# Optimization experiments

Hardware: AMD Instinct MI355X
Metric: run time of the kernel (lower is better)

## Reference

```python
import jax, jax.numpy as jnp
import numpy as np

B, N, K = 4, 2048, 32
CIN, COUT, M = 64, 64, 8
HID = 16
EPS = 1e-5


def setup_inputs() -> dict:
    key = jax.random.key(0)
    ks = jax.random.split(key, 12)
    inp = {
        "grouped_xyz": jax.random.normal(ks[0], (B, 3, N, K), jnp.float32),
        "grouped_dist": jax.random.uniform(ks[1], (B, N, K), jnp.float32),
        "grouped_norm": jax.random.normal(ks[2], (B, 3, N, K), jnp.float32),
        "grouped_angle": jax.random.normal(ks[3], (B, 3, N, K), jnp.float32),
        "feature": jax.random.normal(ks[4], (B, CIN, N, K), jnp.float32),
        # scorenet conv1 (14->16, 1x1, no bias) + BN params
        "w1": jax.random.normal(ks[5], (HID, 14), jnp.float32) * (2.0 / 14) ** 0.5,
        "g1": jnp.ones((HID,), jnp.float32),
        "b1": jnp.zeros((HID,), jnp.float32),
        # scorenet conv2 (16->M, 1x1, with bias, no last bn)
        "w2": jax.random.normal(ks[6], (M, HID), jnp.float32) * (2.0 / HID) ** 0.5,
        "bias2": jnp.zeros((M,), jnp.float32),
        # weight bank: kaiming on (M, CIN, COUT) -> permute -> (CIN, M*COUT)
        "weightbank": (jax.random.normal(ks[7], (M, CIN, COUT), jnp.float32)
                       * (2.0 / CIN) ** 0.5).transpose(1, 0, 2).reshape(CIN, M * COUT),
        # output BN params
        "gamma": jnp.ones((COUT,), jnp.float32),
        "beta": jnp.zeros((COUT,), jnp.float32),
    }
    return inp


def _bn_train(x, gamma, beta):
    # BatchNorm2d in training mode: stats over (B, N, K) per channel (axis=1)
    mean = x.mean(axis=(0, 2, 3), keepdims=True)
    var = x.var(axis=(0, 2, 3), keepdims=True)
    xn = (x - mean) * jax.lax.rsqrt(var + EPS)
    return xn * gamma[None, :, None, None] + beta[None, :, None, None]


def _softmax_one(x, axis):
    # exp(x) / (1 + sum exp(x)), numerically stable
    m = jax.lax.stop_gradient(x.max(axis=axis, keepdims=True))
    e = jnp.exp(x - m)
    return e / (e.sum(axis=axis, keepdims=True) + jnp.exp(-m))


def reference(grouped_xyz, grouped_dist, grouped_norm, grouped_angle, feature,
              w1, g1, b1, w2, bias2, weightbank, gamma, beta):
    # geometric feature build -> (B, 14, N, K)
    center_norm = jnp.broadcast_to(grouped_norm[..., :1], grouped_norm.shape)
    norm_diff = grouped_norm - center_norm
    norm_ed = jnp.linalg.norm(norm_diff, axis=1, keepdims=True)   # (B,1,N,K)
    xyz_ed = jnp.linalg.norm(grouped_xyz, axis=1, keepdims=True)  # (B,1,N,K)
    xyz = jnp.concatenate(
        [grouped_xyz, xyz_ed, grouped_norm, norm_diff, norm_ed, grouped_angle],
        axis=1) / (1.0 + grouped_dist[:, None, :, :])

    # scorenet: 1x1 conv + BN + ReLU, then 1x1 conv + bias, softmax_one over channels
    h = jnp.einsum('oc,bcnk->bonk', w1, xyz)
    h = jax.nn.relu(_bn_train(h, g1, b1))
    s = jnp.einsum('oc,bcnk->bonk', w2, h) + bias2[None, :, None, None]
    scores = _softmax_one(s, axis=1)                 # (B, M, N, K)
    scores = scores.transpose(0, 2, 3, 1)            # (B, N, K, M)

    # weight-bank matmul + score-weighted combine
    feat = feature.transpose(0, 2, 3, 1)             # (B, N, K, CIN)
    out = (feat @ weightbank).reshape(B, N, K, M, COUT)
    out = jnp.einsum('bnkm,bnkmo->bnko', scores, out)  # (B, N, K, COUT)
    out = out.transpose(0, 3, 1, 2)                  # (B, COUT, N, K)

    out = _bn_train(out, gamma, beta)
    return jax.nn.relu(out)
```

## Files before the change

kernel.cpp:

```cpp
#include <hip/hip_runtime.h>
#include <hip/hip_bf16.h>
#include <math.h>

namespace {

constexpr int Kn   = 32;
constexpr int CIN  = 64;
constexpr int COUT = 64;
constexpr int Mn   = 8;
constexpr int HIDn = 16;
constexpr int NK   = 65536;
constexpr int PTOT = 262144;
constexpr float EPSf = 1e-5f;

constexpr int NBLK = 256;
constexpr int NTHR = 1024;

constexpr int WS_SUM1 = 0;
constexpr int WS_SQ1  = 16;
constexpr int WS_SUM2 = 64;
constexpr int WS_SQ2  = 128;
constexpr int WS_BAR  = 192;
constexpr int WS_TOT  = 256;

typedef short bf16x8  __attribute__((ext_vector_type(8)));
typedef float f32x4   __attribute__((ext_vector_type(4)));
typedef float f32x16  __attribute__((ext_vector_type(16)));

__device__ __forceinline__ short f2bf(float f) {
  union { __hip_bfloat16 h; unsigned short u; } cv;
  cv.h = __float2bfloat16(f);
  return (short)cv.u;
}

__device__ __forceinline__ float ws_ld(const float* p) {
  return __hip_atomic_load(p, __ATOMIC_RELAXED, __HIP_MEMORY_SCOPE_AGENT);
}

__device__ __forceinline__ void gridbar(int* cnt, int tid, int target) {
  __syncthreads();
  if (tid == 0) {
    __hip_atomic_fetch_add(cnt, 1, __ATOMIC_ACQ_REL, __HIP_MEMORY_SCOPE_AGENT);
    while (__hip_atomic_load(cnt, __ATOMIC_ACQUIRE,
                             __HIP_MEMORY_SCOPE_AGENT) < target) {
      __builtin_amdgcn_s_sleep(8);
    }
  }
  __syncthreads();
}

__device__ __forceinline__ void geom_h(
    const float* __restrict__ xyz, const float* __restrict__ dist,
    const float* __restrict__ nrm, const float* __restrict__ ang,
    const float* __restrict__ w1, int b, int rem, float h[HIDn]) {
  const int cbase = rem & ~(Kn - 1);
  float x[14];
  const float invd = 1.0f / (1.0f + dist[b * NK + rem]);
  float xe = 0.f, ne = 0.f;
#pragma unroll
  for (int d = 0; d < 3; ++d) {
    const int base = (b * 3 + d) * NK;
    const float gx = xyz[base + rem];
    const float gn = nrm[base + rem];
    const float cn = nrm[base + cbase];
    const float ga = ang[base + rem];
    const float nd = gn - cn;
    x[d] = gx; x[4 + d] = gn; x[7 + d] = nd; x[11 + d] = ga;
    xe += gx * gx; ne += nd * nd;
  }
  x[3]  = sqrtf(xe);
  x[10] = sqrtf(ne);
#pragma unroll
  for (int i = 0; i < 14; ++i) x[i] *= invd;
#pragma unroll
  for (int o = 0; o < HIDn; ++o) {
    float s = 0.f;
#pragma unroll
    for (int c = 0; c < 14; ++c) s = fmaf(w1[o * 14 + c], x[c], s);
    h[o] = s;
  }
}

__global__ __launch_bounds__(512) void k0_zero(float* __restrict__ ws) {
  if (threadIdx.x < WS_TOT) ws[threadIdx.x] = 0.f;
}

__global__ __launch_bounds__(NTHR, 1) void kmain(
    const float* __restrict__ xyz, const float* __restrict__ dist,
    const float* __restrict__ nrm, const float* __restrict__ ang,
    const float* __restrict__ feature, const float* __restrict__ w1,
    const float* __restrict__ g1, const float* __restrict__ b1,
    const float* __restrict__ w2, const float* __restrict__ bias2,
    const float* __restrict__ wb, const float* __restrict__ gamma,
    const float* __restrict__ beta, float* __restrict__ ws,
    float* __restrict__ out) {
  __shared__ short lds_b[64 * 64 * 8];
  __shared__ unsigned park[16 * NTHR];
  __shared__ float red[16][128];
  __shared__ float bnp[160];

  int* const bar = (int*)(ws + WS_BAR);

  const int tid = threadIdx.x;
  const int l   = tid & 63;
  const int w   = tid >> 6;
  const int lg  = l >> 5;
  const int col = l & 31;

  const int blk = blockIdx.x;
  const int pos = blk * NTHR + tid;
  const int b   = pos >> 16;
  const int rem = pos & (NK - 1);

#pragma unroll
  for (int ff = 0; ff < 4; ++ff) {
    const int fi = w * 4 + ff;
    const int kk = fi >> 1;
    const int ct = fi & 1;
    const int c  = kk * 2 + lg;
    const int o  = ct * 32 + col;
    bf16x8 frag;
#pragma unroll
    for (int j = 0; j < 8; ++j) frag[j] = f2bf(wb[c * 512 + j * 64 + o]);
    *reinterpret_cast<bf16x8*>(&lds_b[(fi * 64 + l) * 8]) = frag;
  }

  float h[HIDn];
  geom_h(xyz, dist, nrm, ang, w1, b, rem, h);
  {
    float v[32];
#pragma unroll
    for (int i = 0; i < 16; ++i) { v[i] = h[i]; v[16 + i] = h[i] * h[i]; }
#pragma unroll
    for (int off = 32; off >= 1; off >>= 1) {
#pragma unroll
      for (int i = 0; i < 32; ++i) v[i] += __shfl_xor(v[i], off);
    }
    float mv = 0.f;
#pragma unroll
    for (int i = 0; i < 32; ++i) { if (l == i) mv = v[i]; }
    if (l < 32) red[w][l] = mv;
    __syncthreads();
    if (tid < 32) {
      float tot = 0.f;
#pragma unroll
      for (int ww = 0; ww < 16; ++ww) tot += red[ww][tid];
      atomicAdd(&ws[WS_SUM1 + tid], tot);
    }
  }

  gridbar(bar, tid, NBLK);

  if (tid < HIDn) {
    const float inv  = 1.0f / (float)PTOT;
    const float mean = ws_ld(&ws[WS_SUM1 + tid]) * inv;
    const float var  = ws_ld(&ws[WS_SQ1 + tid]) * inv - mean * mean;
    const float s    = g1[tid] * rsqrtf(var + EPSf);
    bnp[tid]      = s;
    bnp[16 + tid] = b1[tid] - mean * s;
  }
  __syncthreads();

  unsigned scp[4];
  {
#pragma unroll
    for (int o = 0; o < HIDn; ++o)
      h[o] = fmaxf(fmaf(h[o], bnp[o], bnp[16 + o]), 0.f);
    float s[Mn];
#pragma unroll
    for (int m = 0; m < Mn; ++m) {
      float a = bias2[m];
#pragma unroll
      for (int j = 0; j < HIDn; ++j) a = fmaf(w2[m * HIDn + j], h[j], a);
      s[m] = a;
    }
    float mx = s[0];
#pragma unroll
    for (int m = 1; m < Mn; ++m) mx = fmaxf(mx, s[m]);
    float sc[Mn];
    float ssum = 0.f;
#pragma unroll
    for (int m = 0; m < Mn; ++m) { sc[m] = expf(s[m] - mx); ssum += sc[m]; }
    const float inv = 1.0f / (ssum + expf(-mx));
#pragma unroll
    for (int m = 0; m < Mn; ++m) sc[m] *= inv;
#pragma unroll
    for (int j = 0; j < 4; ++j) {
      scp[j] = (unsigned)(unsigned short)f2bf(sc[2 * j]) |
               ((unsigned)(unsigned short)f2bf(sc[2 * j + 1]) << 16);
    }
  }

  const int wrem = (blk * NTHR + w * 64) & (NK - 1);
  const float* fbase = feature + (size_t)b * CIN * NK + wrem;
  f32x16 acc0, acc1;

#pragma unroll
  for (int grp = 0; grp < 2; ++grp) {
    unsigned s0p[4];
#pragma unroll
    for (int j = 0; j < 4; ++j) s0p[j] = __shfl(scp[j], grp * 32 + col);
#pragma unroll
    for (int i = 0; i < 16; ++i) { acc0[i] = 0.f; acc1[i] = 0.f; }

    const float* fp = fbase + (size_t)lg * NK + grp * 32 + col;
#pragma unroll 4
    for (int kk = 0; kk < 32; ++kk) {
      const float fA = *fp;
      fp += 2 * NK;
      bf16x8 a;
#pragma unroll
      for (int j = 0; j < 4; ++j) {
        const float slo = __uint_as_float(s0p[j] << 16);
        const float shi = __uint_as_float(s0p[j] & 0xffff0000u);
        a[2 * j]     = f2bf(fA * slo);
        a[2 * j + 1] = f2bf(fA * shi);
      }
      const bf16x8 b0 =
          *reinterpret_cast<const bf16x8*>(&lds_b[((kk * 2 + 0) * 64 + l) * 8]);
      const bf16x8 b1 =
          *reinterpret_cast<const bf16x8*>(&lds_b[((kk * 2 + 1) * 64 + l) * 8]);
      acc0 = __builtin_amdgcn_mfma_f32_32x32x16_bf16(a, b0, acc0, 0, 0, 0);
      acc1 = __builtin_amdgcn_mfma_f32_32x32x16_bf16(a, b1, acc1, 0, 0, 0);
    }

    {
      float s0s = 0.f, q0s = 0.f, s1s = 0.f, q1s = 0.f;
#pragma unroll
      for (int i = 0; i < 16; ++i) {
        s0s += acc0[i]; q0s += acc0[i] * acc0[i];
        s1s += acc1[i]; q1s += acc1[i] * acc1[i];
      }
      s0s += __shfl_xor(s0s, 32); q0s += __shfl_xor(q0s, 32);
      s1s += __shfl_xor(s1s, 32); q1s += __shfl_xor(q1s, 32);
      if (l < 32) {
        if (grp == 0) {
          red[w][col]      = s0s; red[w][32 + col] = s1s;
          red[w][64 + col] = q0s; red[w][96 + col] = q1s;
        } else {
          red[w][col]      += s0s; red[w][32 + col] += s1s;
          red[w][64 + col] += q0s; red[w][96 + col] += q1s;
        }
      }
    }

    if (grp == 0) {
#pragma unroll
      for (int i = 0; i < 8; ++i) {
        const unsigned w0 =
            (unsigned)(unsigned short)f2bf(acc0[2 * i]) |
            ((unsigned)(unsigned short)f2bf(acc0[2 * i + 1]) << 16);
        const unsigned w1 =
            (unsigned)(unsigned short)f2bf(acc1[2 * i]) |
            ((unsigned)(unsigned short)f2bf(acc1[2 * i + 1]) << 16);
        park[i * NTHR + tid]       = w0;
        park[(8 + i) * NTHR + tid] = w1;
      }
    }
  }

  __syncthreads();
  if (tid < 128) {
    float tot = 0.f;
#pragma unroll
    for (int ww = 0; ww < 16; ++ww) tot += red[ww][tid];
    atomicAdd(&ws[WS_SUM2 + tid], tot);
  }

  gridbar(bar, tid, 2 * NBLK);

  if (tid < COUT) {
    const float inv  = 1.0f / (float)PTOT;
    const float mean = ws_ld(&ws[WS_SUM2 + tid]) * inv;
    const float var  = ws_ld(&ws[WS_SQ2 + tid]) * inv - mean * mean;
    const float s    = gamma[tid] * rsqrtf(var + EPSf);
    bnp[32 + tid] = s;
    bnp[96 + tid] = beta[tid] - mean * s;
  }
  __syncthreads();

  float* obase = out + (size_t)b * COUT * NK + wrem;
#pragma unroll
  for (int ct = 0; ct < 2; ++ct) {
    const int o = ct * 32 + col;
    const float scl = bnp[32 + o];
    const float sh  = bnp[96 + o];
    float* orow = obase + (size_t)o * NK;
#pragma unroll
    for (int q = 0; q < 4; ++q) {
      f32x4 v1;
#pragma unroll
      for (int i = 0; i < 4; ++i) {
        const float vv = ct ? acc1[q * 4 + i] : acc0[q * 4 + i];
        v1[i] = fmaxf(fmaf(vv, scl, sh), 0.f);
      }
      *reinterpret_cast<f32x4*>(&orow[32 + q * 8 + 4 * lg]) = v1;
      const unsigned wa = park[(ct * 8 + q * 2 + 0) * NTHR + tid];
      const unsigned wb2 = park[(ct * 8 + q * 2 + 1) * NTHR + tid];
      f32x4 v0;
      v0[0] = __uint_as_float(wa << 16);
      v0[1] = __uint_as_float(wa & 0xffff0000u);
      v0[2] = __uint_as_float(wb2 << 16);
      v0[3] = __uint_as_float(wb2 & 0xffff0000u);
#pragma unroll
      for (int i = 0; i < 4; ++i) v0[i] = fmaxf(fmaf(v0[i], scl, sh), 0.f);
      *reinterpret_cast<f32x4*>(&orow[q * 8 + 4 * lg]) = v0;
    }
  }
}

}

extern "C" void kernel_launch(void* const* d_in, const int* in_sizes, int n_in,
                              void* d_out, int out_size, void* d_ws, size_t ws_size,
                              hipStream_t stream) {
  const float* xyz     = (const float*)d_in[0];
  const float* dist    = (const float*)d_in[1];
  const float* nrm     = (const float*)d_in[2];
  const float* ang     = (const float*)d_in[3];
  const float* feature = (const float*)d_in[4];
  const float* w1      = (const float*)d_in[5];
  const float* g1      = (const float*)d_in[6];
  const float* b1      = (const float*)d_in[7];
  const float* w2      = (const float*)d_in[8];
  const float* bias2   = (const float*)d_in[9];
  const float* wb      = (const float*)d_in[10];
  const float* gamma   = (const float*)d_in[11];
  const float* beta    = (const float*)d_in[12];
  float* out = (float*)d_out;
  float* ws  = (float*)d_ws;

  hipLaunchKernelGGL(k0_zero, dim3(1), dim3(512), 0, stream, ws);
  hipLaunchKernelGGL(kmain, dim3(NBLK), dim3(NTHR), 0, stream,
                     xyz, dist, nrm, ang, feature, w1, g1, b1,
                     w2, bias2, wb, gamma, beta, ws, out);
}
```

Before: 84.24 us.

## Replicate grid-barrier counters and BN stat slots; stage output stores through LDS

Batch-norm statistics and the grid-barrier counter are spread over 8 replicas, chosen by block index. This cuts contention on single atomic addresses, at the cost of summing the replicas after each barrier. Output tiles are written into a per-wave padded LDS staging buffer, then read back transposed, so each store instruction writes 32 consecutive floats of one output row instead of scattered 16-byte chunks. Shared memory becomes one manually carved buffer, and the staging area reuses the weight and reduction regions once they are no longer needed. The f32x4 writes into the stride-33 staging buffer may not be 16-byte aligned.

```diff
diff --git a/kernel.cpp b/kernel.cpp
--- a/kernel.cpp
+++ b/kernel.cpp
@@ -15,13 +15,9 @@
 
 constexpr int NBLK = 256;
 constexpr int NTHR = 1024;
-
-constexpr int WS_SUM1 = 0;
-constexpr int WS_SQ1  = 16;
-constexpr int WS_SUM2 = 64;
-constexpr int WS_SQ2  = 128;
-constexpr int WS_BAR  = 192;
-constexpr int WS_TOT  = 256;
+constexpr int NREP = 8;
+
+constexpr int WS_ZERO = 4096;
 
 typedef short bf16x8  __attribute__((ext_vector_type(8)));
 typedef float f32x4   __attribute__((ext_vector_type(4)));
@@ -37,14 +33,22 @@
   return __hip_atomic_load(p, __ATOMIC_RELAXED, __HIP_MEMORY_SCOPE_AGENT);
 }
 
-__device__ __forceinline__ void gridbar(int* cnt, int tid, int target) {
+__device__ __forceinline__ void gridbar(float* ws, int blk, int tid,
+                                        int target) {
+  int* cnt = (int*)(ws + 2048);
   __syncthreads();
   if (tid == 0) {
-    __hip_atomic_fetch_add(cnt, 1, __ATOMIC_ACQ_REL, __HIP_MEMORY_SCOPE_AGENT);
-    while (__hip_atomic_load(cnt, __ATOMIC_ACQUIRE,
-                             __HIP_MEMORY_SCOPE_AGENT) < target) {
-      __builtin_amdgcn_s_sleep(8);
-    }
+    __hip_atomic_fetch_add(&cnt[(blk & (NREP - 1)) * 16], 1, __ATOMIC_ACQ_REL,
+                           __HIP_MEMORY_SCOPE_AGENT);
+    int s;
+    do {
+      s = 0;
+#pragma unroll
+      for (int i = 0; i < NREP; ++i)
+        s += __hip_atomic_load(&cnt[i * 16], __ATOMIC_ACQUIRE,
+                               __HIP_MEMORY_SCOPE_AGENT);
+      if (s < target) __builtin_amdgcn_s_sleep(8);
+    } while (s < target);
   }
   __syncthreads();
 }
@@ -82,7 +86,7 @@
 }
 
 __global__ __launch_bounds__(512) void k0_zero(float* __restrict__ ws) {
-  if (threadIdx.x < WS_TOT) ws[threadIdx.x] = 0.f;
+  for (int i = threadIdx.x; i < WS_ZERO; i += 512) ws[i] = 0.f;
 }
 
 __global__ __launch_bounds__(NTHR, 1) void kmain(
@@ -94,12 +98,11 @@
     const float* __restrict__ wb, const float* __restrict__ gamma,
     const float* __restrict__ beta, float* __restrict__ ws,
     float* __restrict__ out) {
-  __shared__ short lds_b[64 * 64 * 8];
-  __shared__ unsigned park[16 * NTHR];
-  __shared__ float red[16][128];
-  __shared__ float bnp[160];
-
-  int* const bar = (int*)(ws + WS_BAR);
+  __shared__ __align__(16) char smem[139904];
+  unsigned* park = reinterpret_cast<unsigned*>(smem);
+  short*    lds_b = reinterpret_cast<short*>(smem + 65536);
+  float (*red)[128] = reinterpret_cast<float(*)[128]>(smem + 131072);
+  float*    bnp = reinterpret_cast<float*>(smem + 139264);
 
   const int tid = threadIdx.x;
   const int l   = tid & 63;
@@ -108,9 +111,12 @@
   const int col = l & 31;
 
   const int blk = blockIdx.x;
+  const int rep = (blk & (NREP - 1)) * 256;
   const int pos = blk * NTHR + tid;
   const int b   = pos >> 16;
   const int rem = pos & (NK - 1);
+
+  float* stage = reinterpret_cast<float*>(smem + 65536) + w * 1056;
 
 #pragma unroll
   for (int ff = 0; ff < 4; ++ff) {
@@ -145,16 +151,22 @@
       float tot = 0.f;
 #pragma unroll
       for (int ww = 0; ww < 16; ++ww) tot += red[ww][tid];
-      atomicAdd(&ws[WS_SUM1 + tid], tot);
-    }
-  }
-
-  gridbar(bar, tid, NBLK);
+      atomicAdd(&ws[rep + tid], tot);
+    }
+  }
+
+  gridbar(ws, blk, tid, NBLK);
 
   if (tid < HIDn) {
+    float sm = 0.f, sq = 0.f;
+#pragma unroll
+    for (int r = 0; r < NREP; ++r) {
+      sm += ws_ld(&ws[r * 256 + tid]);
+      sq += ws_ld(&ws[r * 256 + 16 + tid]);
+    }
     const float inv  = 1.0f / (float)PTOT;
-    const float mean = ws_ld(&ws[WS_SUM1 + tid]) * inv;
-    const float var  = ws_ld(&ws[WS_SQ1 + tid]) * inv - mean * mean;
+    const float mean = sm * inv;
+    const float var  = sq * inv - mean * mean;
     const float s    = g1[tid] * rsqrtf(var + EPSf);
     bnp[tid]      = s;
     bnp[16 + tid] = b1[tid] - mean * s;
@@ -264,15 +276,21 @@
     float tot = 0.f;
 #pragma unroll
     for (int ww = 0; ww < 16; ++ww) tot += red[ww][tid];
-    atomicAdd(&ws[WS_SUM2 + tid], tot);
-  }
-
-  gridbar(bar, tid, 2 * NBLK);
+    atomicAdd(&ws[rep + 64 + tid], tot);
+  }
+
+  gridbar(ws, blk, tid, 2 * NBLK);
 
   if (tid < COUT) {
+    float sm = 0.f, sq = 0.f;
+#pragma unroll
+    for (int r = 0; r < NREP; ++r) {
+      sm += ws_ld(&ws[r * 256 + 64 + tid]);
+      sq += ws_ld(&ws[r * 256 + 128 + tid]);
+    }
     const float inv  = 1.0f / (float)PTOT;
-    const float mean = ws_ld(&ws[WS_SUM2 + tid]) * inv;
-    const float var  = ws_ld(&ws[WS_SQ2 + tid]) * inv - mean * mean;
+    const float mean = sm * inv;
+    const float var  = sq * inv - mean * mean;
     const float s    = gamma[tid] * rsqrtf(var + EPSf);
     bnp[32 + tid] = s;
     bnp[96 + tid] = beta[tid] - mean * s;
@@ -285,26 +303,38 @@
     const int o = ct * 32 + col;
     const float scl = bnp[32 + o];
     const float sh  = bnp[96 + o];
-    float* orow = obase + (size_t)o * NK;
-#pragma unroll
-    for (int q = 0; q < 4; ++q) {
-      f32x4 v1;
-#pragma unroll
-      for (int i = 0; i < 4; ++i) {
-        const float vv = ct ? acc1[q * 4 + i] : acc0[q * 4 + i];
-        v1[i] = fmaxf(fmaf(vv, scl, sh), 0.f);
-      }
-      *reinterpret_cast<f32x4*>(&orow[32 + q * 8 + 4 * lg]) = v1;
-      const unsigned wa = park[(ct * 8 + q * 2 + 0) * NTHR + tid];
-      const unsigned wb2 = park[(ct * 8 + q * 2 + 1) * NTHR + tid];
-      f32x4 v0;
-      v0[0] = __uint_as_float(wa << 16);
-      v0[1] = __uint_as_float(wa & 0xffff0000u);
-      v0[2] = __uint_as_float(wb2 << 16);
-      v0[3] = __uint_as_float(wb2 & 0xffff0000u);
-#pragma unroll
-      for (int i = 0; i < 4; ++i) v0[i] = fmaxf(fmaf(v0[i], scl, sh), 0.f);
-      *reinterpret_cast<f32x4*>(&orow[q * 8 + 4 * lg]) = v0;
+#pragma unroll
+    for (int grp = 0; grp < 2; ++grp) {
+      if (grp == 1) {
+#pragma unroll
+        for (int q = 0; q < 4; ++q) {
+          f32x4 v;
+#pragma unroll
+          for (int i = 0; i < 4; ++i) {
+            const float vv = ct ? acc1[q * 4 + i] : acc0[q * 4 + i];
+            v[i] = fmaxf(fmaf(vv, scl, sh), 0.f);
+          }
+          *reinterpret_cast<f32x4*>(&stage[col * 33 + q * 8 + 4 * lg]) = v;
+        }
+      } else {
+#pragma unroll
+        for (int i = 0; i < 8; ++i) {
+          const unsigned wd = park[(ct * 8 + i) * NTHR + tid];
+          float lo = __uint_as_float(wd << 16);
+          float hi = __uint_as_float(wd & 0xffff0000u);
+          lo = fmaxf(fmaf(lo, scl, sh), 0.f);
+          hi = fmaxf(fmaf(hi, scl, sh), 0.f);
+          float2 v2 = {lo, hi};
+          *reinterpret_cast<float2*>(
+              &stage[col * 33 + (i >> 1) * 8 + 4 * lg + (i & 1) * 2]) = v2;
+        }
+      }
+#pragma unroll
+      for (int rr = 0; rr < 16; ++rr) {
+        const int orow = rr * 2 + lg;
+        const float vv = stage[orow * 33 + col];
+        obase[(size_t)(ct * 32 + orow) * NK + grp * 32 + col] = vv;
+      }
     }
   }
 }
```

Result: slower. 108.5 us (+28.8%).
